# Kernel tuning notes

Hardware: AMD Instinct MI355X
Metric: run time of the kernel (lower is better)

Reference implementation:

```python
import jax, jax.numpy as jnp
import numpy as np
import math

B, H, N, K, D = 4, 8, 4096, 32, 8  # batch, heads, points, neighbors, head depth (k_out/H)


def setup_inputs() -> dict:
    key = jax.random.key(0)
    ks = jax.random.split(key, 6)
    return {
        "q": jax.random.normal(ks[0], (B, H, N, 1, D), dtype=jnp.float32),
        "k_mat": jax.random.normal(ks[1], (B, H, N, D, K), dtype=jnp.float32),
        "v": jax.random.normal(ks[2], (B, H, N, K, D), dtype=jnp.float32),
        "re_xyz": jax.random.normal(ks[3], (B, N, K, 3), dtype=jnp.float32),
        "w1": jax.random.normal(ks[4], (3, H), dtype=jnp.float32) * 0.5,  # linear1: 3 -> num_heads
        "b1": jnp.zeros((H,), dtype=jnp.float32),
        "w2": jax.random.normal(ks[5], (3, H * D), dtype=jnp.float32) * 0.5,  # linear2: 3 -> k_out
        "b2": jnp.zeros((H * D,), dtype=jnp.float32),
    }


def reference(q, k_mat, v, re_xyz, w1, b1, w2, b2):
    # pe_ii positional bias on attention scores: [B,N,K,3] -> [B,N,K,H] -> [B,H,N,1,K]
    q_xyz = re_xyz @ w1 + b1
    q_xyz = jnp.transpose(q_xyz, (0, 3, 1, 2))[:, :, :, None, :]
    # energy: [B,H,N,1,D] @ [B,H,N,D,K] -> [B,H,N,1,K]
    energy = jnp.matmul(q, k_mat) + q_xyz
    scale = math.sqrt(q.shape[-1])
    attention = jax.nn.softmax(energy / scale, axis=-1)
    # value positional term: [B,N,K,H*D] raw-reshaped to [B,H,N,K,D] (matches torch .view)
    v_xyz = (re_xyz @ w2 + b2).reshape(v.shape[0], H, v.shape[2], v.shape[3], D)
    v = v + v_xyz
    # [B,H,N,1,K] @ [B,H,N,K,D] -> [B,H,N,1,D] -> [B,N,H,D]
    x = jnp.matmul(attention, v)[:, :, :, 0, :].transpose(0, 2, 1, 3)
    return x
```

## Files before the change

### kernel.cpp

```cpp
#include <hip/hip_runtime.h>
#include <math.h>


#define T_PER_BLOCK 8

__global__ __launch_bounds__(256) void pe_attn_kernel(
    const float* __restrict__ q,
    const float* __restrict__ k_mat,
    const float* __restrict__ v,
    const float* __restrict__ re_xyz,
    const float* __restrict__ w1,
    const float* __restrict__ b1,
    const float* __restrict__ w2,
    const float* __restrict__ b2,
    float* __restrict__ out)
{
    __shared__ __align__(16) float lds_k[T_PER_BLOCK * 256];
    __shared__ __align__(16) float lds_q[T_PER_BLOCK * 8];
    __shared__ __align__(16) float lds_w[288];

    const int tid = threadIdx.x;
    const int t0  = blockIdx.x * T_PER_BLOCK;

    {
        const float4* ks = (const float4*)(k_mat + (size_t)t0 * 256);
        float4* kd = (float4*)lds_k;
        kd[tid]       = ks[tid];
        kd[tid + 256] = ks[tid + 256];
        if (tid < 16)
            ((float4*)lds_q)[tid] = ((const float4*)(q + (size_t)t0 * 8))[tid];
        if (tid < 288) {
            int i = tid; float val;
            if (i < 24)       val = w1[i];
            else if (i < 32)  val = b1[i - 24];
            else if (i < 224) val = w2[i - 32];
            else              val = b2[i - 224];
            lds_w[i] = val;
        }
        if (tid < 32) {
            int i = tid + 256;
            lds_w[i] = b2[i - 224];
        }
    }
    __syncthreads();

    const int it  = tid >> 5;
    const int k   = tid & 31;
    const int t   = t0 + it;
    const int b   = t >> 15;
    const int rem = t & 32767;
    const int h   = rem >> 12;
    const int n   = rem & 4095;

    const float4 qa = ((const float4*)lds_q)[it * 2];
    const float4 qb = ((const float4*)lds_q)[it * 2 + 1];
    const float* kt = lds_k + it * 256;
    float e = qa.x * kt[k]
            + qa.y * kt[32  + k]
            + qa.z * kt[64  + k]
            + qa.w * kt[96  + k]
            + qb.x * kt[128 + k]
            + qb.y * kt[160 + k]
            + qb.z * kt[192 + k]
            + qb.w * kt[224 + k];

    const size_t rxb = ((size_t)((b << 12) + n) * 32 + k) * 3;
    const float rx0 = re_xyz[rxb], rx1 = re_xyz[rxb + 1], rx2 = re_xyz[rxb + 2];
    e += rx0 * lds_w[h] + rx1 * lds_w[8 + h] + rx2 * lds_w[16 + h] + lds_w[24 + h];

    e *= 0.35355339059327373f;

    float m = e;
    #pragma unroll
    for (int off = 16; off; off >>= 1) m = fmaxf(m, __shfl_xor(m, off));
    const float p = expf(e - m);
    float s = p;
    #pragma unroll
    for (int off = 16; off; off >>= 1) s += __shfl_xor(s, off);
    const float a = p / s;

    const float* vbase = v + (size_t)t * 256 + k * 8;
    const float4 v0 = ((const float4*)vbase)[0];
    const float4 v1 = ((const float4*)vbase)[1];

    const int n2 = rem >> 3;
    const int k2 = ((rem & 7) << 2) + (k >> 3);
    const size_t rxb2 = ((size_t)((b << 12) + n2) * 32 + k2) * 3;
    const float s0 = re_xyz[rxb2], s1 = re_xyz[rxb2 + 1], s2 = re_xyz[rxb2 + 2];

    const int c0 = (k & 7) << 3;
    const float4 wr0a = ((const float4*)(lds_w + 32 + c0))[0];
    const float4 wr0b = ((const float4*)(lds_w + 32 + c0))[1];
    const float4 wr1a = ((const float4*)(lds_w + 96 + c0))[0];
    const float4 wr1b = ((const float4*)(lds_w + 96 + c0))[1];
    const float4 wr2a = ((const float4*)(lds_w + 160 + c0))[0];
    const float4 wr2b = ((const float4*)(lds_w + 160 + c0))[1];
    const float4 bba  = ((const float4*)(lds_w + 224 + c0))[0];
    const float4 bbb  = ((const float4*)(lds_w + 224 + c0))[1];

    float pd[8];
    pd[0] = a * (v0.x + s0 * wr0a.x + s1 * wr1a.x + s2 * wr2a.x + bba.x);
    pd[1] = a * (v0.y + s0 * wr0a.y + s1 * wr1a.y + s2 * wr2a.y + bba.y);
    pd[2] = a * (v0.z + s0 * wr0a.z + s1 * wr1a.z + s2 * wr2a.z + bba.z);
    pd[3] = a * (v0.w + s0 * wr0a.w + s1 * wr1a.w + s2 * wr2a.w + bba.w);
    pd[4] = a * (v1.x + s0 * wr0b.x + s1 * wr1b.x + s2 * wr2b.x + bbb.x);
    pd[5] = a * (v1.y + s0 * wr0b.y + s1 * wr1b.y + s2 * wr2b.y + bbb.y);
    pd[6] = a * (v1.z + s0 * wr0b.z + s1 * wr1b.z + s2 * wr2b.z + bbb.z);
    pd[7] = a * (v1.w + s0 * wr0b.w + s1 * wr1b.w + s2 * wr2b.w + bbb.w);

    #pragma unroll
    for (int off = 16; off; off >>= 1) {
        #pragma unroll
        for (int d = 0; d < 8; ++d) pd[d] += __shfl_xor(pd[d], off);
    }

    if (k < 8) {
        float a0 = (k & 1) ? pd[1] : pd[0];
        float a1 = (k & 1) ? pd[3] : pd[2];
        float a2 = (k & 1) ? pd[5] : pd[4];
        float a3 = (k & 1) ? pd[7] : pd[6];
        float u0 = (k & 2) ? a1 : a0;
        float u1 = (k & 2) ? a3 : a2;
        float wsel = (k & 4) ? u1 : u0;
        out[((size_t)((b << 12) + n) * 8 + h) * 8 + k] = wsel;
    }
}

extern "C" void kernel_launch(void* const* d_in, const int* in_sizes, int n_in,
                              void* d_out, int out_size, void* d_ws, size_t ws_size,
                              hipStream_t stream) {
    const float* q      = (const float*)d_in[0];
    const float* k_mat  = (const float*)d_in[1];
    const float* v      = (const float*)d_in[2];
    const float* re_xyz = (const float*)d_in[3];
    const float* w1     = (const float*)d_in[4];
    const float* b1     = (const float*)d_in[5];
    const float* w2     = (const float*)d_in[6];
    const float* b2     = (const float*)d_in[7];
    float* out = (float*)d_out;

    dim3 grid(131072 / T_PER_BLOCK), block(256);
    hipLaunchKernelGGL(pe_attn_kernel, grid, block, 0, stream,
                       q, k_mat, v, re_xyz, w1, b1, w2, b2, out);
}
```

Baseline: 288.5 us.

## Replace butterfly all-reduce with recursive-halving shuffles, drop LDS staging and softmax max

The per-dimension full butterfly (40 shuffles) becomes a recursive-halving reduce-scatter, so each lane ends with one output dimension after 9 shuffles. Lanes with k%4==0 write their dimension, scaled by a reciprocal of the exp sum. The LDS staging of k, q and the weights, along with its barrier, is removed in favour of direct global loads. Softmax now skips the max subtraction and uses fast __expf, which cuts a reduction but risks overflow for large energies.

```diff
diff --git a/kernel.cpp b/kernel.cpp
--- a/kernel.cpp
+++ b/kernel.cpp
@@ -15,35 +15,8 @@
     const float* __restrict__ b2,
     float* __restrict__ out)
 {
-    __shared__ __align__(16) float lds_k[T_PER_BLOCK * 256];
-    __shared__ __align__(16) float lds_q[T_PER_BLOCK * 8];
-    __shared__ __align__(16) float lds_w[288];
-
     const int tid = threadIdx.x;
     const int t0  = blockIdx.x * T_PER_BLOCK;
-
-    {
-        const float4* ks = (const float4*)(k_mat + (size_t)t0 * 256);
-        float4* kd = (float4*)lds_k;
-        kd[tid]       = ks[tid];
-        kd[tid + 256] = ks[tid + 256];
-        if (tid < 16)
-            ((float4*)lds_q)[tid] = ((const float4*)(q + (size_t)t0 * 8))[tid];
-        if (tid < 288) {
-            int i = tid; float val;
-            if (i < 24)       val = w1[i];
-            else if (i < 32)  val = b1[i - 24];
-            else if (i < 224) val = w2[i - 32];
-            else              val = b2[i - 224];
-            lds_w[i] = val;
-        }
-        if (tid < 32) {
-            int i = tid + 256;
-            lds_w[i] = b2[i - 224];
-        }
-    }
-    __syncthreads();
-
     const int it  = tid >> 5;
     const int k   = tid & 31;
     const int t   = t0 + it;
@@ -52,77 +25,96 @@
     const int h   = rem >> 12;
     const int n   = rem & 4095;
 
-    const float4 qa = ((const float4*)lds_q)[it * 2];
-    const float4 qb = ((const float4*)lds_q)[it * 2 + 1];
-    const float* kt = lds_k + it * 256;
-    float e = qa.x * kt[k]
-            + qa.y * kt[32  + k]
-            + qa.z * kt[64  + k]
-            + qa.w * kt[96  + k]
-            + qb.x * kt[128 + k]
-            + qb.y * kt[160 + k]
-            + qb.z * kt[192 + k]
-            + qb.w * kt[224 + k];
+    const float* kbase = k_mat + (size_t)t * 256 + k;
+    float kc0 = kbase[0];
+    float kc1 = kbase[32];
+    float kc2 = kbase[64];
+    float kc3 = kbase[96];
+    float kc4 = kbase[128];
+    float kc5 = kbase[160];
+    float kc6 = kbase[192];
+    float kc7 = kbase[224];
+
+    const float4 qa = ((const float4*)(q + (size_t)t * 8))[0];
+    const float4 qb = ((const float4*)(q + (size_t)t * 8))[1];
 
     const size_t rxb = ((size_t)((b << 12) + n) * 32 + k) * 3;
     const float rx0 = re_xyz[rxb], rx1 = re_xyz[rxb + 1], rx2 = re_xyz[rxb + 2];
-    e += rx0 * lds_w[h] + rx1 * lds_w[8 + h] + rx2 * lds_w[16 + h] + lds_w[24 + h];
-
-    e *= 0.35355339059327373f;
-
-    float m = e;
-    #pragma unroll
-    for (int off = 16; off; off >>= 1) m = fmaxf(m, __shfl_xor(m, off));
-    const float p = expf(e - m);
-    float s = p;
-    #pragma unroll
-    for (int off = 16; off; off >>= 1) s += __shfl_xor(s, off);
-    const float a = p / s;
-
-    const float* vbase = v + (size_t)t * 256 + k * 8;
-    const float4 v0 = ((const float4*)vbase)[0];
-    const float4 v1 = ((const float4*)vbase)[1];
 
     const int n2 = rem >> 3;
     const int k2 = ((rem & 7) << 2) + (k >> 3);
     const size_t rxb2 = ((size_t)((b << 12) + n2) * 32 + k2) * 3;
     const float s0 = re_xyz[rxb2], s1 = re_xyz[rxb2 + 1], s2 = re_xyz[rxb2 + 2];
 
+    const float* vbase = v + (size_t)t * 256 + k * 8;
+    const float4 v0 = ((const float4*)vbase)[0];
+    const float4 v1 = ((const float4*)vbase)[1];
+
+    const float wq0 = w1[h], wq1 = w1[8 + h], wq2 = w1[16 + h], bq = b1[h];
     const int c0 = (k & 7) << 3;
-    const float4 wr0a = ((const float4*)(lds_w + 32 + c0))[0];
-    const float4 wr0b = ((const float4*)(lds_w + 32 + c0))[1];
-    const float4 wr1a = ((const float4*)(lds_w + 96 + c0))[0];
-    const float4 wr1b = ((const float4*)(lds_w + 96 + c0))[1];
-    const float4 wr2a = ((const float4*)(lds_w + 160 + c0))[0];
-    const float4 wr2b = ((const float4*)(lds_w + 160 + c0))[1];
-    const float4 bba  = ((const float4*)(lds_w + 224 + c0))[0];
-    const float4 bbb  = ((const float4*)(lds_w + 224 + c0))[1];
+    const float4 wr0a = ((const float4*)(w2 + c0))[0];
+    const float4 wr0b = ((const float4*)(w2 + c0))[1];
+    const float4 wr1a = ((const float4*)(w2 + 64 + c0))[0];
+    const float4 wr1b = ((const float4*)(w2 + 64 + c0))[1];
+    const float4 wr2a = ((const float4*)(w2 + 128 + c0))[0];
+    const float4 wr2b = ((const float4*)(w2 + 128 + c0))[1];
+    const float4 bba  = ((const float4*)(b2 + c0))[0];
+    const float4 bbb  = ((const float4*)(b2 + c0))[1];
+
+    float e = qa.x * kc0 + qa.y * kc1 + qa.z * kc2 + qa.w * kc3
+            + qb.x * kc4 + qb.y * kc5 + qb.z * kc6 + qb.w * kc7;
+    e += rx0 * wq0 + rx1 * wq1 + rx2 * wq2 + bq;
+    e *= 0.35355339059327373f;
+    const float p = __expf(e);
+
+    float s = p;
+    #pragma unroll
+    for (int off = 16; off; off >>= 1) s += __shfl_xor(s, off);
 
     float pd[8];
-    pd[0] = a * (v0.x + s0 * wr0a.x + s1 * wr1a.x + s2 * wr2a.x + bba.x);
-    pd[1] = a * (v0.y + s0 * wr0a.y + s1 * wr1a.y + s2 * wr2a.y + bba.y);
-    pd[2] = a * (v0.z + s0 * wr0a.z + s1 * wr1a.z + s2 * wr2a.z + bba.z);
-    pd[3] = a * (v0.w + s0 * wr0a.w + s1 * wr1a.w + s2 * wr2a.w + bba.w);
-    pd[4] = a * (v1.x + s0 * wr0b.x + s1 * wr1b.x + s2 * wr2b.x + bbb.x);
-    pd[5] = a * (v1.y + s0 * wr0b.y + s1 * wr1b.y + s2 * wr2b.y + bbb.y);
-    pd[6] = a * (v1.z + s0 * wr0b.z + s1 * wr1b.z + s2 * wr2b.z + bbb.z);
-    pd[7] = a * (v1.w + s0 * wr0b.w + s1 * wr1b.w + s2 * wr2b.w + bbb.w);
+    pd[0] = p * (v0.x + s0 * wr0a.x + s1 * wr1a.x + s2 * wr2a.x + bba.x);
+    pd[1] = p * (v0.y + s0 * wr0a.y + s1 * wr1a.y + s2 * wr2a.y + bba.y);
+    pd[2] = p * (v0.z + s0 * wr0a.z + s1 * wr1a.z + s2 * wr2a.z + bba.z);
+    pd[3] = p * (v0.w + s0 * wr0a.w + s1 * wr1a.w + s2 * wr2a.w + bba.w);
+    pd[4] = p * (v1.x + s0 * wr0b.x + s1 * wr1b.x + s2 * wr2b.x + bbb.x);
+    pd[5] = p * (v1.y + s0 * wr0b.y + s1 * wr1b.y + s2 * wr2b.y + bbb.y);
+    pd[6] = p * (v1.z + s0 * wr0b.z + s1 * wr1b.z + s2 * wr2b.z + bbb.z);
+    pd[7] = p * (v1.w + s0 * wr0b.w + s1 * wr1b.w + s2 * wr2b.w + bbb.w);
 
-    #pragma unroll
-    for (int off = 16; off; off >>= 1) {
+    {
+        const bool hb = (k & 16) != 0;
         #pragma unroll
-        for (int d = 0; d < 8; ++d) pd[d] += __shfl_xor(pd[d], off);
+        for (int j = 0; j < 4; ++j) {
+            float send = hb ? pd[j] : pd[j + 4];
+            float recv = __shfl_xor(send, 16);
+            float keep = hb ? pd[j + 4] : pd[j];
+            pd[j] = keep + recv;
+        }
     }
+    {
+        const bool hb = (k & 8) != 0;
+        #pragma unroll
+        for (int j = 0; j < 2; ++j) {
+            float send = hb ? pd[j] : pd[j + 2];
+            float recv = __shfl_xor(send, 8);
+            float keep = hb ? pd[j + 2] : pd[j];
+            pd[j] = keep + recv;
+        }
+    }
+    {
+        const bool hb = (k & 4) != 0;
+        float send = hb ? pd[0] : pd[1];
+        float recv = __shfl_xor(send, 4);
+        float keep = hb ? pd[1] : pd[0];
+        pd[0] = keep + recv;
+    }
+    pd[0] += __shfl_xor(pd[0], 2);
+    pd[0] += __shfl_xor(pd[0], 1);
 
-    if (k < 8) {
-        float a0 = (k & 1) ? pd[1] : pd[0];
-        float a1 = (k & 1) ? pd[3] : pd[2];
-        float a2 = (k & 1) ? pd[5] : pd[4];
-        float a3 = (k & 1) ? pd[7] : pd[6];
-        float u0 = (k & 2) ? a1 : a0;
-        float u1 = (k & 2) ? a3 : a2;
-        float wsel = (k & 4) ? u1 : u0;
-        out[((size_t)((b << 12) + n) * 8 + h) * 8 + k] = wsel;
+    if ((k & 3) == 0) {
+        const int d = (k >> 2) & 7;
+        out[((size_t)((b << 12) + n) * 8 + h) * 8 + d] =
+            pd[0] * __builtin_amdgcn_rcpf(s);
     }
 }
 
```

Result: no change. 286.4 us (-0.7%).
